# Kernel optimization log

Hardware: AMD Instinct MI355X
Metric: run time of the kernel (lower is better)

Reference implementation:

```python
import jax, jax.numpy as jnp
import numpy as np
from jax import lax

WINDOW_SIZE = 11
SIGMA = 1.5
C1 = 0.01 ** 2
C2 = 0.03 ** 2


def _make_window():
    xs = np.arange(WINDOW_SIZE) - WINDOW_SIZE // 2
    g = np.exp(-(xs.astype(np.float32) ** 2) / (2.0 * SIGMA ** 2))
    g = g / g.sum()
    w2d = np.outer(g, g).astype(np.float32)  # (ws, ws)
    return jnp.asarray(w2d)[None, None, :, :]  # (O=1, I=1, ws, ws)


def _blur(x, window):
    pad = WINDOW_SIZE // 2
    return lax.conv_general_dilated(
        x, window,
        window_strides=(1, 1),
        padding=[(pad, pad), (pad, pad)],
        dimension_numbers=("NCHW", "OIHW", "NCHW"),
    )


def setup_inputs() -> dict:
    key = jax.random.key(0)
    k1, k2 = jax.random.split(key)
    shape = (64, 1, 512, 512)
    img1 = jax.random.uniform(k1, shape, dtype=jnp.float32)
    img2 = jax.random.uniform(k2, shape, dtype=jnp.float32)
    return {"img1": img1, "img2": img2}


def reference(img1, img2):
    window = _make_window()
    mu1 = _blur(img1, window)
    mu2 = _blur(img2, window)
    mu1_sq = mu1 * mu1
    mu2_sq = mu2 * mu2
    mu1_mu2 = mu1 * mu2
    sigma1_sq = _blur(img1 * img1, window) - mu1_sq
    sigma2_sq = _blur(img2 * img2, window) - mu2_sq
    sigma12 = _blur(img1 * img2, window) - mu1_mu2
    ssim_map = ((2.0 * mu1_mu2 + C1) * (2.0 * sigma12 + C2)) / (
        (mu1_sq + mu2_sq + C1) * (sigma1_sq + sigma2_sq + C2)
    )
    return ssim_map.mean()  # size_average=True
```

## Files before the change

kernel.cpp:

```cpp
#include <hip/hip_runtime.h>

#define IMG 512
#define HALO 5
#define BAND 16
#define NB 16
#define RING 28

#define W0 1.0283800e-03f
#define W1 7.5987582e-03f
#define W2 3.6000773e-02f
#define W3 1.0936070e-01f
#define W4 2.1300553e-01f
#define W5 2.6601172e-01f

typedef float f2 __attribute__((ext_vector_type(2)));

__device__ __forceinline__ f2 pkfma(f2 a, f2 b, f2 c) {
    return __builtin_elementwise_fma(a, b, c);
}

#define LGKM_BARRIER() asm volatile("s_waitcnt lgkmcnt(0)\n\ts_barrier" ::: "memory")

__global__ __launch_bounds__(256, 4)
void ssim_main(const float* __restrict__ img1, const float* __restrict__ img2,
               float* __restrict__ part)
{
    const float Wt[11] = {W0,W1,W2,W3,W4,W5,W4,W3,W2,W1,W0};
    constexpr float C1 = 1.0e-4f;
    constexpr float C2 = 9.0e-4f;

    __shared__ float4 sH[RING][65];
    __shared__ float  sRed[4];

    const int bx     = blockIdx.x;
    const int n      = bx >> 4;
    const int stripe = (bx >> 1) & 7;
    const int half   = bx & 1;
    const int gx0    = stripe << 6;
    const int base   = half << 8;
    const int tid    = threadIdx.x;
    const bool edge  = (stripe == 0) | (stripe == 7);

    const float* __restrict__ base1 = img1 + (size_t)n * IMG * IMG;
    const float* __restrict__ base2 = img2 + (size_t)n * IMG * IMG;

    float acc = 0.0f;

    auto loadRowP = [&](const float* r1, const float* r2, bool rok, int gcb,
                        float4* px, float4* py) {
        #pragma unroll
        for (int t = 0; t < 5; ++t) {
            int gc = gcb - 8 + (t << 2);
            bool ok = rok && (gc >= 0) && (gc < IMG);
            px[t] = ok ? ((const float4*)r1)[t] : make_float4(0.f,0.f,0.f,0.f);
            py[t] = ok ? ((const float4*)r2)[t] : make_float4(0.f,0.f,0.f,0.f);
        }
    };

    auto horizStore = [&](const float4* px, const float4* py, int slot, int cg) {
        const int c0 = cg << 2;
        float X[20], Y[20];
        #pragma unroll
        for (int t = 0; t < 5; ++t) {
            X[4*t+0]=px[t].x; X[4*t+1]=px[t].y; X[4*t+2]=px[t].z; X[4*t+3]=px[t].w;
            Y[4*t+0]=py[t].x; Y[4*t+1]=py[t].y; Y[4*t+2]=py[t].z; Y[4*t+3]=py[t].w;
        }
        f2 xy[14], sp[14];
        #pragma unroll
        for (int j = 0; j < 14; ++j) {
            float x = X[3+j], y = Y[3+j];
            xy[j] = f2{x, y};
            sp[j] = f2{fmaf(x, x, y*y), x*y};
        }
        #pragma unroll
        for (int o = 0; o < 4; ++o) {
            f2 m = {0.f, 0.f}, t2 = {0.f, 0.f};
            #pragma unroll
            for (int k = 0; k < 11; ++k) {
                f2 w2 = {Wt[k], Wt[k]};
                m  = pkfma(w2, xy[o+k], m);
                t2 = pkfma(w2, sp[o+k], t2);
            }
            sH[slot][c0+o] = make_float4(m.x, m.y, t2.x, t2.y);
        }
    };

    for (int task = tid; task < 26 * 16; task += 256) {
        int i   = task >> 4;
        int cg  = task & 15;
        int gr  = base - HALO + i;
        int gcb = gx0 + (cg << 2);
        const float* r1 = base1 + (ptrdiff_t)gr * IMG + gcb - 8;
        const float* r2 = base2 + (ptrdiff_t)gr * IMG + gcb - 8;
        float4 px[5], py[5];
        loadRowP(r1, r2, (unsigned)gr < (unsigned)IMG, gcb, px, py);
        horizStore(px, py, i, cg);
    }

    const int rr  = tid >> 4;
    const int cgs = tid & 15;
    const int gcb = gx0 + (cgs << 2);
    const float* p1 = base1 + (ptrdiff_t)(base + 21 + rr) * IMG + gcb - 8;
    const float* p2 = base2 + (ptrdiff_t)(base + 21 + rr) * IMG + gcb - 8;

    int sb = 0;
    for (int b = 0; b < NB; ++b) {
        float4 px[5], py[5];
        const bool pf = (b + 1 < NB);
        if (pf) {
            const bool rowsafe = (half == 0) | (b < 14);
            if (rowsafe & (!edge)) {
                #pragma unroll
                for (int t = 0; t < 5; ++t) {
                    px[t] = ((const float4*)p1)[t];
                    py[t] = ((const float4*)p2)[t];
                }
            } else {
                int gr = base + (b << 4) + 21 + rr;
                loadRowP(p1, p2, (unsigned)gr < (unsigned)IMG, gcb, px, py);
            }
        }

        LGKM_BARRIER();

        {
            const int wv  = __builtin_amdgcn_readfirstlane(tid >> 6);
            const int col = tid & 63;
            const int d0  = sb + (wv << 2);
            f2 a[14], p[14];
            #pragma unroll
            for (int i = 0; i < 14; ++i) {
                int s = d0 + i;
                s -= (s >= RING) ? RING : 0;
                s -= (s >= RING) ? RING : 0;
                float4 q = sH[s][col];
                a[i] = f2{q.x, q.y};
                p[i] = f2{q.z, q.w};
            }
            #pragma unroll
            for (int q4 = 0; q4 < 4; ++q4) {
                f2 m = {0.f,0.f}, tt = {0.f,0.f};
                #pragma unroll
                for (int k = 0; k < 11; ++k) {
                    f2 w2 = {Wt[k], Wt[k]};
                    m  = pkfma(w2, a[q4+k], m);
                    tt = pkfma(w2, p[q4+k], tt);
                }
                f2 msq     = m * m;
                float mu12  = m.x * m.y;
                float musum = msq.x + msq.y;
                float g12   = tt.y - mu12;
                float gs    = tt.x - musum;
                float num = fmaf(2.f, mu12, C1) * fmaf(2.f, g12, C2);
                float den = (musum + C1) * (gs + C2);
                acc = fmaf(num, __builtin_amdgcn_rcpf(den), acc);
            }
        }

        LGKM_BARRIER();

        if (pf) {
            int t = sb + 26 + rr;
            t -= (t >= RING) ? RING : 0;
            t -= (t >= RING) ? RING : 0;
            horizStore(px, py, t, cgs);
            p1 += BAND * IMG;
            p2 += BAND * IMG;
        }
        sb += BAND;
        sb -= (sb >= RING) ? RING : 0;
    }

    #pragma unroll
    for (int off = 32; off > 0; off >>= 1)
        acc += __shfl_down(acc, off, 64);
    if ((tid & 63) == 0) sRed[tid >> 6] = acc;
    LGKM_BARRIER();
    if (tid == 0) part[bx] = sRed[0] + sRed[1] + sRed[2] + sRed[3];
}

__global__ void ssim_finalize(const float* __restrict__ part, float* __restrict__ out)
{
    double s = 0.0;
    const int t = threadIdx.x;
    for (int i = t; i < 1024; i += 64) s += (double)part[i];
    #pragma unroll
    for (int off = 32; off > 0; off >>= 1)
        s += __shfl_down(s, off, 64);
    if (t == 0) out[0] = (float)(s * (1.0 / 16777216.0));
}

extern "C" void kernel_launch(void* const* d_in, const int* in_sizes, int n_in,
                              void* d_out, int out_size, void* d_ws, size_t ws_size,
                              hipStream_t stream)
{
    const float* img1 = (const float*)d_in[0];
    const float* img2 = (const float*)d_in[1];
    float* out  = (float*)d_out;
    float* part = (float*)d_ws;

    ssim_main<<<1024, 256, 0, stream>>>(img1, img2, part);
    ssim_finalize<<<1, 64, 0, stream>>>(part, out);
}
```

Measured before the change: 175.8 us.

## Split image rows into quarters, shrink LDS ring, stream FMAs, swizzle LDS columns

Each block now handles a 128-row quarter instead of a 256-row half, which doubles the grid to 2048 blocks and raises the occupancy hint to 5. The LDS ring drops to 26 rows with an XOR column swizzle in place of padding, so shared memory per block shrinks and bank conflicts stay low. The horizontal and vertical blur loops are rewritten to accumulate directly from each loaded element rather than staging arrays, which lowers register pressure. The finalize kernel is widened to 256 threads for the larger partial array. The cost is more halo rows recomputed per output row.

```diff
diff --git a/kernel.cpp b/kernel.cpp
--- a/kernel.cpp
+++ b/kernel.cpp
@@ -3,8 +3,8 @@
 #define IMG 512
 #define HALO 5
 #define BAND 16
-#define NB 16
-#define RING 28
+#define NB 8
+#define RING 26
 
 #define W0 1.0283800e-03f
 #define W1 7.5987582e-03f
@@ -21,7 +21,7 @@
 
 #define LGKM_BARRIER() asm volatile("s_waitcnt lgkmcnt(0)\n\ts_barrier" ::: "memory")
 
-__global__ __launch_bounds__(256, 4)
+__global__ __launch_bounds__(256, 5)
 void ssim_main(const float* __restrict__ img1, const float* __restrict__ img2,
                float* __restrict__ part)
 {
@@ -29,17 +29,17 @@
     constexpr float C1 = 1.0e-4f;
     constexpr float C2 = 9.0e-4f;
 
-    __shared__ float4 sH[RING][65];
+    __shared__ float4 sH[RING][64];
     __shared__ float  sRed[4];
 
-    const int bx     = blockIdx.x;
-    const int n      = bx >> 4;
-    const int stripe = (bx >> 1) & 7;
-    const int half   = bx & 1;
-    const int gx0    = stripe << 6;
-    const int base   = half << 8;
-    const int tid    = threadIdx.x;
-    const bool edge  = (stripe == 0) | (stripe == 7);
+    const int bx      = blockIdx.x;
+    const int n       = bx >> 5;
+    const int stripe  = (bx >> 2) & 7;
+    const int quarter = bx & 3;
+    const int gx0     = stripe << 6;
+    const int base    = quarter << 7;
+    const int tid     = threadIdx.x;
+    const bool edge   = (stripe == 0) | (stripe == 7);
 
     const float* __restrict__ base1 = img1 + (size_t)n * IMG * IMG;
     const float* __restrict__ base2 = img2 + (size_t)n * IMG * IMG;
@@ -58,42 +58,54 @@
     };
 
     auto horizStore = [&](const float4* px, const float4* py, int slot, int cg) {
-        const int c0 = cg << 2;
-        float X[20], Y[20];
+        f2 m[4]  = {f2{0.f,0.f},f2{0.f,0.f},f2{0.f,0.f},f2{0.f,0.f}};
+        f2 t2[4] = {f2{0.f,0.f},f2{0.f,0.f},f2{0.f,0.f},f2{0.f,0.f}};
         #pragma unroll
         for (int t = 0; t < 5; ++t) {
-            X[4*t+0]=px[t].x; X[4*t+1]=px[t].y; X[4*t+2]=px[t].z; X[4*t+3]=px[t].w;
-            Y[4*t+0]=py[t].x; Y[4*t+1]=py[t].y; Y[4*t+2]=py[t].z; Y[4*t+3]=py[t].w;
-        }
-        f2 xy[14], sp[14];
-        #pragma unroll
-        for (int j = 0; j < 14; ++j) {
-            float x = X[3+j], y = Y[3+j];
-            xy[j] = f2{x, y};
-            sp[j] = f2{fmaf(x, x, y*y), x*y};
-        }
+            #pragma unroll
+            for (int e = 0; e < 4; ++e) {
+                const int j = (t << 2) + e;
+                if (j < 3 || j > 16) continue;
+                const float x = (e==0) ? px[t].x : (e==1) ? px[t].y : (e==2) ? px[t].z : px[t].w;
+                const float y = (e==0) ? py[t].x : (e==1) ? py[t].y : (e==2) ? py[t].z : py[t].w;
+                const f2 v  = {x, y};
+                const f2 s2 = {fmaf(x, x, y*y), x*y};
+                #pragma unroll
+                for (int o = 0; o < 4; ++o) {
+                    const int k = j - 3 - o;
+                    if (0 <= k && k <= 10) {
+                        const f2 w = {Wt[k], Wt[k]};
+                        m[o]  = pkfma(w, v,  m[o]);
+                        t2[o] = pkfma(w, s2, t2[o]);
+                    }
+                }
+            }
+        }
+        const int c4 = cg << 2;
         #pragma unroll
         for (int o = 0; o < 4; ++o) {
-            f2 m = {0.f, 0.f}, t2 = {0.f, 0.f};
-            #pragma unroll
-            for (int k = 0; k < 11; ++k) {
-                f2 w2 = {Wt[k], Wt[k]};
-                m  = pkfma(w2, xy[o+k], m);
-                t2 = pkfma(w2, sp[o+k], t2);
-            }
-            sH[slot][c0+o] = make_float4(m.x, m.y, t2.x, t2.y);
+            const int wc = (c4 + o) ^ cg;
+            sH[slot][wc] = make_float4(m[o].x, m[o].y, t2[o].x, t2[o].y);
         }
     };
 
-    for (int task = tid; task < 26 * 16; task += 256) {
-        int i   = task >> 4;
-        int cg  = task & 15;
-        int gr  = base - HALO + i;
-        int gcb = gx0 + (cg << 2);
+    for (int task = tid; task < RING * 16; task += 256) {
+        const int i   = task >> 4;
+        const int cg  = task & 15;
+        const int gr  = base - HALO + i;
+        const int gcb = gx0 + (cg << 2);
         const float* r1 = base1 + (ptrdiff_t)gr * IMG + gcb - 8;
         const float* r2 = base2 + (ptrdiff_t)gr * IMG + gcb - 8;
         float4 px[5], py[5];
-        loadRowP(r1, r2, (unsigned)gr < (unsigned)IMG, gcb, px, py);
+        if (!edge && gr >= 0) {
+            #pragma unroll
+            for (int t = 0; t < 5; ++t) {
+                px[t] = ((const float4*)r1)[t];
+                py[t] = ((const float4*)r2)[t];
+            }
+        } else {
+            loadRowP(r1, r2, gr >= 0, gcb, px, py);
+        }
         horizStore(px, py, i, cg);
     }
 
@@ -103,12 +115,16 @@
     const float* p1 = base1 + (ptrdiff_t)(base + 21 + rr) * IMG + gcb - 8;
     const float* p2 = base2 + (ptrdiff_t)(base + 21 + rr) * IMG + gcb - 8;
 
+    const int col  = tid & 63;
+    const int rcol = col ^ (col >> 2);
+    const int wv   = __builtin_amdgcn_readfirstlane(tid >> 6);
+
     int sb = 0;
     for (int b = 0; b < NB; ++b) {
         float4 px[5], py[5];
         const bool pf = (b + 1 < NB);
         if (pf) {
-            const bool rowsafe = (half == 0) | (b < 14);
+            const bool rowsafe = (quarter < 3) | (b < NB - 2);
             if (rowsafe & (!edge)) {
                 #pragma unroll
                 for (int t = 0; t < 5; ++t) {
@@ -116,7 +132,7 @@
                     py[t] = ((const float4*)p2)[t];
                 }
             } else {
-                int gr = base + (b << 4) + 21 + rr;
+                const int gr = base + (b << 4) + 21 + rr;
                 loadRowP(p1, p2, (unsigned)gr < (unsigned)IMG, gcb, px, py);
             }
         }
@@ -124,35 +140,37 @@
         LGKM_BARRIER();
 
         {
-            const int wv  = __builtin_amdgcn_readfirstlane(tid >> 6);
-            const int col = tid & 63;
-            const int d0  = sb + (wv << 2);
-            f2 a[14], p[14];
+            const int d0 = sb + (wv << 2);
+            f2 ma[4] = {f2{0.f,0.f},f2{0.f,0.f},f2{0.f,0.f},f2{0.f,0.f}};
+            f2 sa[4] = {f2{0.f,0.f},f2{0.f,0.f},f2{0.f,0.f},f2{0.f,0.f}};
             #pragma unroll
             for (int i = 0; i < 14; ++i) {
                 int s = d0 + i;
                 s -= (s >= RING) ? RING : 0;
-                s -= (s >= RING) ? RING : 0;
-                float4 q = sH[s][col];
-                a[i] = f2{q.x, q.y};
-                p[i] = f2{q.z, q.w};
-            }
-            #pragma unroll
-            for (int q4 = 0; q4 < 4; ++q4) {
-                f2 m = {0.f,0.f}, tt = {0.f,0.f};
+                const float4 q = sH[s][rcol];
+                const f2 v = {q.x, q.y};
+                const f2 u = {q.z, q.w};
                 #pragma unroll
-                for (int k = 0; k < 11; ++k) {
-                    f2 w2 = {Wt[k], Wt[k]};
-                    m  = pkfma(w2, a[q4+k], m);
-                    tt = pkfma(w2, p[q4+k], tt);
+                for (int o = 0; o < 4; ++o) {
+                    const int k = i - o;
+                    if (0 <= k && k <= 10) {
+                        const f2 w = {Wt[k], Wt[k]};
+                        ma[o] = pkfma(w, v, ma[o]);
+                        sa[o] = pkfma(w, u, sa[o]);
+                    }
                 }
-                f2 msq     = m * m;
-                float mu12  = m.x * m.y;
-                float musum = msq.x + msq.y;
-                float g12   = tt.y - mu12;
-                float gs    = tt.x - musum;
-                float num = fmaf(2.f, mu12, C1) * fmaf(2.f, g12, C2);
-                float den = (musum + C1) * (gs + C2);
+            }
+            #pragma unroll
+            for (int o = 0; o < 4; ++o) {
+                const f2 m   = ma[o];
+                const f2 tt  = sa[o];
+                const f2 msq = m * m;
+                const float mu12  = m.x * m.y;
+                const float musum = msq.x + msq.y;
+                const float g12 = tt.y - mu12;
+                const float gs  = tt.x - musum;
+                const float num = fmaf(2.f, mu12, C1) * fmaf(2.f, g12, C2);
+                const float den = (musum + C1) * (gs + C2);
                 acc = fmaf(num, __builtin_amdgcn_rcpf(den), acc);
             }
         }
@@ -160,8 +178,7 @@
         LGKM_BARRIER();
 
         if (pf) {
-            int t = sb + 26 + rr;
-            t -= (t >= RING) ? RING : 0;
+            int t = sb + rr;
             t -= (t >= RING) ? RING : 0;
             horizStore(px, py, t, cgs);
             p1 += BAND * IMG;
@@ -181,13 +198,16 @@
 
 __global__ void ssim_finalize(const float* __restrict__ part, float* __restrict__ out)
 {
+    __shared__ double sD[4];
     double s = 0.0;
     const int t = threadIdx.x;
-    for (int i = t; i < 1024; i += 64) s += (double)part[i];
+    for (int i = t; i < 2048; i += 256) s += (double)part[i];
     #pragma unroll
     for (int off = 32; off > 0; off >>= 1)
         s += __shfl_down(s, off, 64);
-    if (t == 0) out[0] = (float)(s * (1.0 / 16777216.0));
+    if ((t & 63) == 0) sD[t >> 6] = s;
+    __syncthreads();
+    if (t == 0) out[0] = (float)((sD[0] + sD[1] + sD[2] + sD[3]) * (1.0 / 16777216.0));
 }
 
 extern "C" void kernel_launch(void* const* d_in, const int* in_sizes, int n_in,
@@ -199,6 +219,6 @@
     float* out  = (float*)d_out;
     float* part = (float*)d_ws;
 
-    ssim_main<<<1024, 256, 0, stream>>>(img1, img2, part);
-    ssim_finalize<<<1, 64, 0, stream>>>(part, out);
-}
+    ssim_main<<<2048, 256, 0, stream>>>(img1, img2, part);
+    ssim_finalize<<<1, 256, 0, stream>>>(part, out);
+}
```

Result: faster. 170.1 us (-3.3%).
